# Performance work log

Hardware: AMD Instinct MI355X
Metric: run time of the kernel (lower is better)

## Reference

```python
import jax, jax.numpy as jnp
import numpy as np

N_NODES = 80000
N_EDGES = 1280000
D_NODE = 128
D_EDGE = 32
HID = 64
OUT = 32
EPS_GEN = 1e-7
EPS_BN = 1e-5


def _lin_init(key, fan_in, fan_out):
    return (jax.random.normal(key, (fan_in, fan_out), jnp.float32) / np.sqrt(fan_in))


def setup_inputs() -> dict:
    key = jax.random.key(0)
    ks = jax.random.split(key, 20)
    inp = {
        "x": jax.random.normal(ks[0], (N_NODES, D_NODE), jnp.float32),
        "edge_index": jax.random.randint(ks[1], (2, N_EDGES), 0, N_NODES, jnp.int32),
        "edge_attr": jax.random.normal(ks[2], (N_EDGES, D_EDGE), jnp.float32),
        # encoders
        "node_W": _lin_init(ks[3], D_NODE, HID), "node_b": jnp.zeros((HID,), jnp.float32),
        "edge_W": _lin_init(ks[4], D_EDGE, HID), "edge_b": jnp.zeros((HID,), jnp.float32),
        # GENConv layer 1 MLP: [HID -> 2HID (bias=False)] -> BN -> ReLU -> [2HID -> HID (bias=False)]
        "c1_W1": _lin_init(ks[5], HID, 2 * HID), "c1_g": jnp.ones((2 * HID,), jnp.float32), "c1_be": jnp.zeros((2 * HID,), jnp.float32), "c1_W2": _lin_init(ks[6], 2 * HID, HID),
        # GENConv layer 2
        "c2_W1": _lin_init(ks[7], HID, 2 * HID), "c2_g": jnp.ones((2 * HID,), jnp.float32), "c2_be": jnp.zeros((2 * HID,), jnp.float32), "c2_W2": _lin_init(ks[8], 2 * HID, HID),
        # edge update linears on concat(3*HID)
        "l1_W": _lin_init(ks[9], 3 * HID, HID), "l1_b": jnp.zeros((HID,), jnp.float32),
        "l2_W": _lin_init(ks[10], 3 * HID, OUT), "l2_b": jnp.zeros((OUT,), jnp.float32),
    }
    return inp


def _scatter_softmax_agg(msg, dst, n_nodes):
    # SoftmaxAggregation with t=1: per-destination, per-feature softmax weights
    m = jax.ops.segment_max(msg, dst, num_segments=n_nodes)  # [N, H]
    m = jnp.where(jnp.isfinite(m), m, 0.0)                   # nodes w/o in-edges
    ex = jnp.exp(msg - m[dst])                               # [E, H]
    denom = jax.ops.segment_sum(ex, dst, num_segments=n_nodes)
    alpha = ex / (denom[dst] + 1e-16)
    return jax.ops.segment_sum(msg * alpha, dst, num_segments=n_nodes)


def _batchnorm(h, gamma, beta):
    mu = jnp.mean(h, axis=0)
    var = jnp.var(h, axis=0)
    return (h - mu) * jax.lax.rsqrt(var + EPS_BN) * gamma + beta


def _genconv(x, src, dst, edge_attr, W1, g, be, W2):
    msg = jax.nn.relu(x[src] + edge_attr) + EPS_GEN          # [E, HID]
    agg = _scatter_softmax_agg(msg, dst, x.shape[0])         # [N, HID]
    h = agg + x
    h = jax.nn.relu(_batchnorm(h @ W1, g, be))
    return h @ W2


def reference(x, edge_index, edge_attr, node_W, node_b, edge_W, edge_b,
              c1_W1, c1_g, c1_be, c1_W2, c2_W1, c2_g, c2_be, c2_W2,
              l1_W, l1_b, l2_W, l2_b):
    src, dst = edge_index[0], edge_index[1]
    ea = edge_attr @ edge_W + edge_b                          # [E, HID]
    h = x @ node_W + node_b                                   # [N, HID]

    convs = [(c1_W1, c1_g, c1_be, c1_W2), (c2_W1, c2_g, c2_be, c2_W2)]
    lins = [(l1_W, l1_b), (l2_W, l2_b)]
    for (W1, g, be, W2), (lW, lb) in zip(convs, lins):
        h = jax.nn.relu(_genconv(h, src, dst, ea, W1, g, be, W2))
        # dropout is identity in eval mode
        ef = jnp.concatenate([h[src], ea, h[dst]], axis=-1)   # [E, 3*HID]
        ea = ef @ lW + lb
    return h, ea
```

## Files before the change

### kernel.cpp

```cpp
#include <hip/hip_runtime.h>
#include <hip/hip_bf16.h>

#define N_NODES 80000
#define N_EDGES 1280000
constexpr int DN = 128;
constexpr int DE = 32;
constexpr int H  = 64;
constexpr int H2 = 128;
constexpr float EPS_GEN = 1e-7f;
constexpr float EPS_BN  = 1e-5f;

typedef _Float16 f16x8 __attribute__((ext_vector_type(8)));
typedef _Float16 f16x4 __attribute__((ext_vector_type(4)));
typedef float f32x4 __attribute__((ext_vector_type(4)));

__device__ __forceinline__ void atomAddF(float* p, float v) {
  __hip_atomic_fetch_add(p, v, __ATOMIC_RELAXED, __HIP_MEMORY_SCOPE_AGENT);
}

struct PrepDesc { const float* W; _Float16* img; int K; int OC; int blkStart; };
struct PrepAll { PrepDesc d[8]; };

__global__ void k_prep_all(PrepAll P) {
  int b = blockIdx.x;
  int i = 0;
#pragma unroll
  for (int t = 1; t < 8; ++t)
    if (P.d[t].blkStart <= b) i = t;
  const PrepDesc D = P.d[i];
  int idx = (b - D.blkStart) * 256 + threadIdx.x;
  if (idx >= D.K * D.OC) return;
  int nslabK = D.K >> 5;
  int j = idx & 7, m16 = (idx >> 3) & 15, kg = (idx >> 7) & 3;
  int slab = idx >> 9;
  int kk = slab % nslabK, n2 = slab / nslabK;
  int k = kk * 32 + kg * 8 + j, n = n2 * 16 + m16;
  D.img[idx] = (_Float16)D.W[k * D.OC + n];
}

template <int K, int OC, bool IN16, bool AFFINE, bool BIAS,
          bool RELU_OUT, bool OUT16, bool OUT32, bool CLRS, bool SCATOUT>
__global__ __launch_bounds__(256) void k_dense(
    const void* __restrict__ Ain, const _Float16* __restrict__ wimg,
    const float* __restrict__ bias, const float* __restrict__ sums,
    const float* __restrict__ g, const float* __restrict__ be,
    const int* __restrict__ posmap,
    _Float16* __restrict__ out16, float* __restrict__ out32,
    float* __restrict__ sums_clr) {
  constexpr int NK = K / 32, NF = OC / 16;
  __shared__ float sSC[H2], sSH[H2];
  const int tid = threadIdx.x, wv = tid >> 6, lane = tid & 63;
  const int m16 = lane & 15, kg = lane >> 4;
  const int rowbase = blockIdx.x * 64 + wv * 16;
  if constexpr (CLRS) {
    if (blockIdx.x == 0) sums_clr[tid] = 0.0f;
  }
  if constexpr (AFFINE) {
    for (int i = tid; i < H2; i += 256) {
      float mu  = sums[i] * (1.0f / N_NODES);
      float var = sums[H2 + i] * (1.0f / N_NODES) - mu * mu;
      float sc  = rsqrtf(var + EPS_BN) * g[i];
      sSC[i] = sc;
      sSH[i] = be[i] - mu * sc;
    }
    __syncthreads();
  }
  const int arow = rowbase + m16;
  f32x4 acc[NF];
#pragma unroll
  for (int n2 = 0; n2 < NF; ++n2) {
    float bv = BIAS ? bias[n2 * 16 + m16] : 0.0f;
    acc[n2] = (f32x4){bv, bv, bv, bv};
  }
  const _Float16* wp = wimg + (size_t)lane * 8;
#pragma unroll
  for (int kk = 0; kk < NK; ++kk) {
    f16x8 a;
    if constexpr (IN16) {
      const _Float16* ap = (const _Float16*)Ain + (size_t)arow * K + kg * 8 + kk * 32;
      a = *(const f16x8*)ap;
      if constexpr (AFFINE) {
#pragma unroll
        for (int j = 0; j < 8; ++j) {
          int f = kg * 8 + kk * 32 + j;
          float v = fmaxf(fmaf((float)a[j], sSC[f], sSH[f]), 0.0f);
          a[j] = (_Float16)v;
        }
      }
    } else {
      const float* ap = (const float*)Ain + (size_t)arow * K + kg * 8 + kk * 32;
      float4 v0 = *(const float4*)ap;
      float4 v1 = *(const float4*)(ap + 4);
      a = (f16x8){(_Float16)v0.x, (_Float16)v0.y, (_Float16)v0.z, (_Float16)v0.w,
                  (_Float16)v1.x, (_Float16)v1.y, (_Float16)v1.z, (_Float16)v1.w};
    }
#pragma unroll
    for (int n2 = 0; n2 < NF; ++n2) {
      f16x8 bb = *(const f16x8*)(wp + ((size_t)(n2 * NK + kk) << 9));
      acc[n2] = __builtin_amdgcn_mfma_f32_16x16x32_f16(a, bb, acc[n2], 0, 0, 0);
    }
  }
#pragma unroll
  for (int n2 = 0; n2 < NF; ++n2)
#pragma unroll
    for (int r = 0; r < 4; ++r) {
      float o = acc[n2][r];
      if constexpr (RELU_OUT) o = fmaxf(o, 0.0f);
      int orow = rowbase + kg * 4 + r;
      if constexpr (SCATOUT) orow = posmap[orow];
      size_t oi = (size_t)orow * OC + n2 * 16 + m16;
      if constexpr (OUT16) out16[oi] = (_Float16)o;
      if constexpr (OUT32) out32[oi] = o;
    }
}

template <int OC, typename OUT_T, int T, bool SCAT>
__global__ __launch_bounds__(256) void k_edge_upd_srt(
    const _Float16* __restrict__ h, const _Float16* __restrict__ ea,
    const int2* __restrict__ eids, const int* __restrict__ dstS,
    const _Float16* __restrict__ wimg, const float* __restrict__ lb,
    OUT_T* __restrict__ eout) {
  constexpr int NF = OC / 16;
  __shared__ _Float16 sWf[NF * 6 * 512];
  __shared__ int sS[T * 64], sD[T * 64];
  __shared__ int sE[SCAT ? T * 64 : 1];
  const int tid = threadIdx.x, wv = tid >> 6, lane = tid & 63;
  const int m16 = lane & 15, kg = lane >> 4;
  const int p0 = blockIdx.x * (T * 64);

  for (int i = tid; i < T * 64; i += 256) {
    int2 t = eids[p0 + i];
    sS[i] = t.y;
    sD[i] = dstS[p0 + i];
    if constexpr (SCAT) sE[i] = t.x;
  }
  {
    const float4* s4 = (const float4*)wimg;
    float4* d4 = (float4*)sWf;
    constexpr int NV = NF * 6 * 512 / 8;
    for (int i = tid; i < NV; i += 256) d4[i] = s4[i];
  }
  __syncthreads();
  const _Float16* wp = sWf + (size_t)lane * 8;

  float bias_[NF];
#pragma unroll
  for (int n2 = 0; n2 < NF; ++n2) bias_[n2] = lb[n2 * 16 + m16];

  f16x8 FA[6], FB[6];
  auto LOADA = [&](f16x8* F, int l) {
    const _Float16* a0 = h + (size_t)sS[l] * H + kg * 8;
    const _Float16* a1 = ea + (size_t)(p0 + l) * H + kg * 8;
    const _Float16* a2 = h + (size_t)sD[l] * H + kg * 8;
    F[0] = *(const f16x8*)a0;
    F[1] = *(const f16x8*)(a0 + 32);
    F[2] = *(const f16x8*)a1;
    F[3] = *(const f16x8*)(a1 + 32);
    F[4] = *(const f16x8*)a2;
    F[5] = *(const f16x8*)(a2 + 32);
  };
  auto COMPUTE = [&](const f16x8* F, int l) {
    f32x4 acc[NF];
#pragma unroll
    for (int n2 = 0; n2 < NF; ++n2)
      acc[n2] = (f32x4){bias_[n2], bias_[n2], bias_[n2], bias_[n2]};
#pragma unroll
    for (int kk = 0; kk < 6; ++kk)
#pragma unroll
      for (int n2 = 0; n2 < NF; ++n2) {
        f16x8 bb = *(const f16x8*)(wp + ((n2 * 6 + kk) << 9));
        acc[n2] = __builtin_amdgcn_mfma_f32_16x16x32_f16(F[kk], bb, acc[n2], 0, 0, 0);
      }
    const int lbase = l - m16;
#pragma unroll
    for (int n2 = 0; n2 < NF; ++n2)
#pragma unroll
      for (int r = 0; r < 4; ++r) {
        int lr = lbase + kg * 4 + r;
        int col = n2 * 16 + m16;
        if constexpr (SCAT)
          eout[(size_t)sE[lr] * OC + col] = (OUT_T)acc[n2][r];
        else
          eout[(size_t)(p0 + lr) * OC + col] = (OUT_T)acc[n2][r];
      }
  };

  const int l0 = wv * 16 + m16;
  LOADA(FA, l0);
  if (T > 1) LOADA(FB, l0 + 64);
#pragma unroll
  for (int t = 0; t < T; ++t) {
    if (t & 1) {
      COMPUTE(FB, l0 + t * 64);
      if (t + 2 < T) LOADA(FB, l0 + (t + 2) * 64);
    } else {
      COMPUTE(FA, l0 + t * 64);
      if (t + 2 < T) LOADA(FA, l0 + (t + 2) * 64);
    }
  }
}

__global__ void k_hist(const int* __restrict__ dst, int* cnt) {
  int e = blockIdx.x * blockDim.x + threadIdx.x;
  if (e < N_EDGES) atomicAdd(&cnt[dst[e]], 1);
}

__global__ void k_scan_blk(const int* __restrict__ cnt, int* __restrict__ bsum) {
  __shared__ int sh[256];
  int i = blockIdx.x * 256 + threadIdx.x;
  sh[threadIdx.x] = (i < N_NODES) ? cnt[i] : 0;
  __syncthreads();
  for (int s = 128; s > 0; s >>= 1) {
    if (threadIdx.x < s) sh[threadIdx.x] += sh[threadIdx.x + s];
    __syncthreads();
  }
  if (threadIdx.x == 0) bsum[blockIdx.x] = sh[0];
}

__global__ void k_scan_top(int* bsum, int nb) {
  __shared__ int sh[512];
  int t = threadIdx.x;
  int orig = (t < nb) ? bsum[t] : 0;
  sh[t] = orig;
  __syncthreads();
  for (int off = 1; off < 512; off <<= 1) {
    int v = (t >= off) ? sh[t - off] : 0;
    __syncthreads();
    sh[t] += v;
    __syncthreads();
  }
  if (t < nb) bsum[t] = sh[t] - orig;
}

__global__ void k_scan_fin(const int* __restrict__ cnt, const int* __restrict__ bsum,
                           int* __restrict__ start, int* __restrict__ cursor) {
  __shared__ int sh[256];
  int i = blockIdx.x * 256 + threadIdx.x;
  int t = threadIdx.x;
  int orig = (i < N_NODES) ? cnt[i] : 0;
  sh[t] = orig;
  __syncthreads();
  for (int off = 1; off < 256; off <<= 1) {
    int v = (t >= off) ? sh[t - off] : 0;
    __syncthreads();
    sh[t] += v;
    __syncthreads();
  }
  if (i < N_NODES) {
    int st = bsum[blockIdx.x] + sh[t] - orig;
    start[i] = st;
    cursor[i] = st;
  }
}

__global__ void k_scatter(const int* __restrict__ src, const int* __restrict__ dst,
                          int* cursor, int2* __restrict__ eids, int* __restrict__ dstS,
                          int* __restrict__ posOf) {
  int e = blockIdx.x * blockDim.x + threadIdx.x;
  if (e < N_EDGES) {
    int d = dst[e];
    int pos = atomicAdd(&cursor[d], 1);
    eids[pos] = make_int2(e, src[e]);
    dstS[pos] = d;
    posOf[e] = pos;
  }
}

__global__ __launch_bounds__(256) void k_agg_csr(
    const _Float16* __restrict__ h, const _Float16* __restrict__ ea_s,
    const int2* __restrict__ eids, const int* __restrict__ start,
    const int* __restrict__ cnt, _Float16* __restrict__ hsum) {
  const int lane = threadIdx.x & 63;
  const int wid  = (int)((blockIdx.x * blockDim.x + threadIdx.x) >> 6);
  if (wid >= N_NODES) return;
  const int ep = lane >> 3, fg = lane & 7;
  const int s0 = start[wid], c = cnt[wid];
  float num[8] = {0.f, 0.f, 0.f, 0.f, 0.f, 0.f, 0.f, 0.f};
  float den[8] = {0.f, 0.f, 0.f, 0.f, 0.f, 0.f, 0.f, 0.f};
  if (c > 0) {
    const int nit = (c + 7) >> 3;
    int idx = min(ep, c - 1);
    f16x8 hA = *(const f16x8*)(h + (size_t)eids[s0 + idx].y * H + fg * 8);
    f16x8 eA = *(const f16x8*)(ea_s + (size_t)(s0 + idx) * H + fg * 8);
    bool vA = (ep < c);
    f16x8 hB = hA, eB = eA;
    bool vB = false;
    if (nit > 1) {
      idx = min(8 + ep, c - 1);
      hB = *(const f16x8*)(h + (size_t)eids[s0 + idx].y * H + fg * 8);
      eB = *(const f16x8*)(ea_s + (size_t)(s0 + idx) * H + fg * 8);
      vB = (8 + ep < c);
    }
    for (int i = 0; i < nit; ++i) {
      f16x8 hc = hA, ec = eA;
      bool vc = vA;
      hA = hB; eA = eB; vA = vB;
      if (i + 2 < nit) {
        idx = min((i + 2) * 8 + ep, c - 1);
        hB = *(const f16x8*)(h + (size_t)eids[s0 + idx].y * H + fg * 8);
        eB = *(const f16x8*)(ea_s + (size_t)(s0 + idx) * H + fg * 8);
        vB = ((i + 2) * 8 + ep < c);
      }
#pragma unroll
      for (int j = 0; j < 8; ++j) {
        float m = fmaxf((float)hc[j] + (float)ec[j], 0.0f) + EPS_GEN;
        float ex = vc ? __expf(m) : 0.0f;
        num[j] = fmaf(m, ex, num[j]);
        den[j] += ex;
      }
    }
  }
#pragma unroll
  for (int j = 0; j < 8; ++j) {
    num[j] += __shfl_xor(num[j], 8);
    num[j] += __shfl_xor(num[j], 16);
    num[j] += __shfl_xor(num[j], 32);
    den[j] += __shfl_xor(den[j], 8);
    den[j] += __shfl_xor(den[j], 16);
    den[j] += __shfl_xor(den[j], 32);
  }
  if (ep == 0) {
    f16x8 hs = *(const f16x8*)(h + (size_t)wid * H + fg * 8);
    f16x8 o;
#pragma unroll
    for (int j = 0; j < 8; ++j)
      o[j] = (_Float16)(num[j] / (den[j] + 1e-16f) + (float)hs[j]);
    *(f16x8*)(hsum + (size_t)wid * H + fg * 8) = o;
  }
}

__global__ void k_bnstats(const _Float16* __restrict__ h3, float* sums) {
  int f = threadIdx.x & (H2 - 1);
  int half = threadIdx.x >> 7;
  float s = 0.0f, q = 0.0f;
  for (int n = blockIdx.x * 2 + half; n < N_NODES; n += gridDim.x * 2) {
    float v = (float)h3[(size_t)n * H2 + f];
    s += v;
    q = fmaf(v, v, q);
  }
  __shared__ float sh[2][2][H2];
  sh[0][half][f] = s;
  sh[1][half][f] = q;
  __syncthreads();
  if (threadIdx.x < H2) {
    atomAddF(&sums[f], sh[0][0][f] + sh[0][1][f]);
    atomAddF(&sums[H2 + f], sh[1][0][f] + sh[1][1][f]);
  }
}

extern "C" void kernel_launch(void* const* d_in, const int* in_sizes, int n_in,
                              void* d_out, int out_size, void* d_ws, size_t ws_size,
                              hipStream_t stream) {
  (void)in_sizes; (void)n_in; (void)out_size; (void)ws_size;
  const float* x      = (const float*)d_in[0];
  const int*   eidx   = (const int*)d_in[1];
  const float* eattr  = (const float*)d_in[2];
  const float* node_W = (const float*)d_in[3];
  const float* node_b = (const float*)d_in[4];
  const float* edge_W = (const float*)d_in[5];
  const float* edge_b = (const float*)d_in[6];
  const float* c1_W1  = (const float*)d_in[7];
  const float* c1_g   = (const float*)d_in[8];
  const float* c1_be  = (const float*)d_in[9];
  const float* c1_W2  = (const float*)d_in[10];
  const float* c2_W1  = (const float*)d_in[11];
  const float* c2_g   = (const float*)d_in[12];
  const float* c2_be  = (const float*)d_in[13];
  const float* c2_W2  = (const float*)d_in[14];
  const float* l1_W   = (const float*)d_in[15];
  const float* l1_b   = (const float*)d_in[16];
  const float* l2_W   = (const float*)d_in[17];
  const float* l2_b   = (const float*)d_in[18];

  const int* src = eidx;
  const int* dst = eidx + N_EDGES;

  char* wsb = (char*)d_ws;
  size_t off = 0;
  _Float16* ea_s  = (_Float16*)(wsb + off); off += (size_t)N_EDGES * H * 2;
  _Float16* hA16  = (_Float16*)(wsb + off); off += (size_t)N_NODES * H * 2;
  _Float16* hB16  = (_Float16*)(wsb + off); off += (size_t)N_NODES * H * 2;
  _Float16* hC16  = (_Float16*)(wsb + off); off += (size_t)N_NODES * H * 2;
  _Float16* hsum16= (_Float16*)(wsb + off); off += (size_t)N_NODES * H * 2;
  _Float16* h3    = (_Float16*)(wsb + off); off += (size_t)N_NODES * H2 * 2;
  float* sums     = (float*)(wsb + off);    off += 256 * 4;
  int* cnt        = (int*)(wsb + off);      off += (size_t)N_NODES * 4;
  int* startA     = (int*)(wsb + off);      off += (size_t)N_NODES * 4;
  int* cursor     = (int*)(wsb + off);      off += (size_t)N_NODES * 4;
  int* bsum       = (int*)(wsb + off);      off += 512 * 4;
  int2* eids      = (int2*)(wsb + off);     off += (size_t)N_EDGES * 8;
  int* dstS       = (int*)(wsb + off);      off += (size_t)N_EDGES * 4;
  int* posOf      = (int*)(wsb + off);      off += (size_t)N_EDGES * 4;
  _Float16* wE    = (_Float16*)(wsb + off); off += DE * H * 2;
  _Float16* wN    = (_Float16*)(wsb + off); off += DN * H * 2;
  _Float16* w1a   = (_Float16*)(wsb + off); off += H * H2 * 2;
  _Float16* w1b   = (_Float16*)(wsb + off); off += H * H2 * 2;
  _Float16* w2a   = (_Float16*)(wsb + off); off += H2 * H * 2;
  _Float16* w2b   = (_Float16*)(wsb + off); off += H2 * H * 2;
  _Float16* wL1   = (_Float16*)(wsb + off); off += 3 * H * H * 2;
  _Float16* wL2   = (_Float16*)(wsb + off); off += 3 * H * 32 * 2;

  float* h_out  = (float*)d_out;
  float* ea_out = (float*)d_out + (size_t)N_NODES * H;

  constexpr int NB = (N_NODES + 255) / 256;

  PrepAll P;
  P.d[0] = {edge_W, wE, DE, H, 0};
  P.d[1] = {node_W, wN, DN, H, 8};
  P.d[2] = {c1_W1, w1a, H, H2, 40};
  P.d[3] = {c2_W1, w1b, H, H2, 72};
  P.d[4] = {c1_W2, w2a, H2, H, 104};
  P.d[5] = {c2_W2, w2b, H2, H, 136};
  P.d[6] = {l1_W, wL1, 192, H, 168};
  P.d[7] = {l2_W, wL2, 192, 32, 216};
  k_prep_all<<<240, 256, 0, stream>>>(P);

  hipMemsetAsync(cnt, 0, N_NODES * 4, stream);
  k_hist<<<(N_EDGES + 255) / 256, 256, 0, stream>>>(dst, cnt);
  k_scan_blk<<<NB, 256, 0, stream>>>(cnt, bsum);
  k_scan_top<<<1, 512, 0, stream>>>(bsum, NB);
  k_scan_fin<<<NB, 256, 0, stream>>>(cnt, bsum, startA, cursor);
  k_scatter<<<(N_EDGES + 255) / 256, 256, 0, stream>>>(src, dst, cursor, eids, dstS, posOf);

  k_dense<DE, H, false, false, true, false, true, false, false, true>
      <<<N_EDGES / 64, 256, 0, stream>>>(eattr, wE, edge_b, nullptr, nullptr, nullptr,
                                         posOf, ea_s, nullptr, nullptr);
  k_dense<DN, H, false, false, true, false, true, false, false, false>
      <<<N_NODES / 64, 256, 0, stream>>>(x, wN, node_b, nullptr, nullptr, nullptr,
                                         nullptr, hA16, nullptr, nullptr);

  k_agg_csr<<<(N_NODES + 3) / 4, 256, 0, stream>>>(hA16, ea_s, eids, startA, cnt, hsum16);
  k_dense<H, H2, true, false, false, false, true, false, true, false>
      <<<N_NODES / 64, 256, 0, stream>>>(hsum16, w1a, nullptr, nullptr, nullptr, nullptr,
                                         nullptr, h3, nullptr, sums);
  k_bnstats<<<1280, 256, 0, stream>>>(h3, sums);
  k_dense<H2, H, true, true, false, true, true, false, false, false>
      <<<N_NODES / 64, 256, 0, stream>>>(h3, w2a, nullptr, sums, c1_g, c1_be,
                                         nullptr, hB16, nullptr, nullptr);
  k_edge_upd_srt<64, _Float16, 8, false>
      <<<N_EDGES / 512, 256, 0, stream>>>(hB16, ea_s, eids, dstS, wL1, l1_b, ea_s);

  k_agg_csr<<<(N_NODES + 3) / 4, 256, 0, stream>>>(hB16, ea_s, eids, startA, cnt, hsum16);
  k_dense<H, H2, true, false, false, false, true, false, true, false>
      <<<N_NODES / 64, 256, 0, stream>>>(hsum16, w1b, nullptr, nullptr, nullptr, nullptr,
                                         nullptr, h3, nullptr, sums);
  k_bnstats<<<1280, 256, 0, stream>>>(h3, sums);
  k_dense<H2, H, true, true, false, true, true, true, false, false>
      <<<N_NODES / 64, 256, 0, stream>>>(h3, w2b, nullptr, sums, c2_g, c2_be,
                                         nullptr, hC16, h_out, nullptr);
  k_edge_upd_srt<32, float, 8, true>
      <<<N_EDGES / 512, 256, 0, stream>>>(hC16, ea_s, eids, dstS, wL2, l2_b, ea_out);
}
```

Before: 685.4 us.

## Fuse BatchNorm statistics into first GEMM and pack edge ids into int4

After: 663.9 us. -3.1%, faster.

```diff
diff --git a/kernel.cpp b/kernel.cpp
--- a/kernel.cpp
+++ b/kernel.cpp
@@ -39,22 +39,20 @@
 }
 
 template <int K, int OC, bool IN16, bool AFFINE, bool BIAS,
-          bool RELU_OUT, bool OUT16, bool OUT32, bool CLRS, bool SCATOUT>
+          bool RELU_OUT, bool OUT16, bool OUT32, bool SCATOUT, bool STATS>
 __global__ __launch_bounds__(256) void k_dense(
     const void* __restrict__ Ain, const _Float16* __restrict__ wimg,
     const float* __restrict__ bias, const float* __restrict__ sums,
     const float* __restrict__ g, const float* __restrict__ be,
     const int* __restrict__ posmap,
     _Float16* __restrict__ out16, float* __restrict__ out32,
-    float* __restrict__ sums_clr) {
+    float* __restrict__ sums_out) {
   constexpr int NK = K / 32, NF = OC / 16;
-  __shared__ float sSC[H2], sSH[H2];
+  __shared__ float sSC[AFFINE ? H2 : 1], sSH[AFFINE ? H2 : 1];
+  __shared__ float sStat[STATS ? 1024 : 1];
   const int tid = threadIdx.x, wv = tid >> 6, lane = tid & 63;
   const int m16 = lane & 15, kg = lane >> 4;
   const int rowbase = blockIdx.x * 64 + wv * 16;
-  if constexpr (CLRS) {
-    if (blockIdx.x == 0) sums_clr[tid] = 0.0f;
-  }
   if constexpr (AFFINE) {
     for (int i = tid; i < H2; i += 256) {
       float mu  = sums[i] * (1.0f / N_NODES);
@@ -112,12 +110,34 @@
       if constexpr (OUT16) out16[oi] = (_Float16)o;
       if constexpr (OUT32) out32[oi] = o;
     }
+  if constexpr (STATS) {
+    static_assert(!STATS || NF == 8, "STATS assumes OC==128");
+#pragma unroll
+    for (int n2 = 0; n2 < NF; ++n2) {
+      float s = acc[n2][0] + acc[n2][1] + acc[n2][2] + acc[n2][3];
+      float q = acc[n2][0] * acc[n2][0] + acc[n2][1] * acc[n2][1] +
+                acc[n2][2] * acc[n2][2] + acc[n2][3] * acc[n2][3];
+      s += __shfl_xor(s, 16); s += __shfl_xor(s, 32);
+      q += __shfl_xor(q, 16); q += __shfl_xor(q, 32);
+      if (kg == 0) {
+        sStat[wv * 128 + n2 * 16 + m16] = s;
+        sStat[512 + wv * 128 + n2 * 16 + m16] = q;
+      }
+    }
+    __syncthreads();
+    {
+      int which = tid >> 7, f = tid & 127;
+      const float* b0 = sStat + which * 512;
+      float v = b0[f] + b0[128 + f] + b0[256 + f] + b0[384 + f];
+      atomAddF(&sums_out[which * H2 + f], v);
+    }
+  }
 }
 
 template <int OC, typename OUT_T, int T, bool SCAT>
 __global__ __launch_bounds__(256) void k_edge_upd_srt(
     const _Float16* __restrict__ h, const _Float16* __restrict__ ea,
-    const int2* __restrict__ eids, const int* __restrict__ dstS,
+    const int4* __restrict__ eidsQ,
     const _Float16* __restrict__ wimg, const float* __restrict__ lb,
     OUT_T* __restrict__ eout) {
   constexpr int NF = OC / 16;
@@ -129,9 +149,9 @@
   const int p0 = blockIdx.x * (T * 64);
 
   for (int i = tid; i < T * 64; i += 256) {
-    int2 t = eids[p0 + i];
+    int4 t = eidsQ[p0 + i];
     sS[i] = t.y;
-    sD[i] = dstS[p0 + i];
+    sD[i] = t.z;
     if constexpr (SCAT) sE[i] = t.x;
   }
   {
@@ -254,22 +274,23 @@
 }
 
 __global__ void k_scatter(const int* __restrict__ src, const int* __restrict__ dst,
-                          int* cursor, int2* __restrict__ eids, int* __restrict__ dstS,
-                          int* __restrict__ posOf) {
+                          int* cursor, int4* __restrict__ eidsQ, int* __restrict__ posOf) {
   int e = blockIdx.x * blockDim.x + threadIdx.x;
   if (e < N_EDGES) {
     int d = dst[e];
+    int s = src[e];
     int pos = atomicAdd(&cursor[d], 1);
-    eids[pos] = make_int2(e, src[e]);
-    dstS[pos] = d;
+    eidsQ[pos] = make_int4(e, s, d, 0);
     posOf[e] = pos;
   }
 }
 
 __global__ __launch_bounds__(256) void k_agg_csr(
     const _Float16* __restrict__ h, const _Float16* __restrict__ ea_s,
-    const int2* __restrict__ eids, const int* __restrict__ start,
-    const int* __restrict__ cnt, _Float16* __restrict__ hsum) {
+    const int4* __restrict__ eidsQ, const int* __restrict__ start,
+    const int* __restrict__ cnt, _Float16* __restrict__ hsum,
+    float* __restrict__ sums_clr) {
+  if (blockIdx.x == 0) sums_clr[threadIdx.x] = 0.0f;
   const int lane = threadIdx.x & 63;
   const int wid  = (int)((blockIdx.x * blockDim.x + threadIdx.x) >> 6);
   if (wid >= N_NODES) return;
@@ -280,14 +301,16 @@
   if (c > 0) {
     const int nit = (c + 7) >> 3;
     int idx = min(ep, c - 1);
-    f16x8 hA = *(const f16x8*)(h + (size_t)eids[s0 + idx].y * H + fg * 8);
+    int2 pe = *(const int2*)(eidsQ + s0 + idx);
+    f16x8 hA = *(const f16x8*)(h + (size_t)pe.y * H + fg * 8);
     f16x8 eA = *(const f16x8*)(ea_s + (size_t)(s0 + idx) * H + fg * 8);
     bool vA = (ep < c);
     f16x8 hB = hA, eB = eA;
     bool vB = false;
     if (nit > 1) {
       idx = min(8 + ep, c - 1);
-      hB = *(const f16x8*)(h + (size_t)eids[s0 + idx].y * H + fg * 8);
+      pe = *(const int2*)(eidsQ + s0 + idx);
+      hB = *(const f16x8*)(h + (size_t)pe.y * H + fg * 8);
       eB = *(const f16x8*)(ea_s + (size_t)(s0 + idx) * H + fg * 8);
       vB = (8 + ep < c);
     }
@@ -297,7 +320,8 @@
       hA = hB; eA = eB; vA = vB;
       if (i + 2 < nit) {
         idx = min((i + 2) * 8 + ep, c - 1);
-        hB = *(const f16x8*)(h + (size_t)eids[s0 + idx].y * H + fg * 8);
+        pe = *(const int2*)(eidsQ + s0 + idx);
+        hB = *(const f16x8*)(h + (size_t)pe.y * H + fg * 8);
         eB = *(const f16x8*)(ea_s + (size_t)(s0 + idx) * H + fg * 8);
         vB = ((i + 2) * 8 + ep < c);
       }
@@ -326,25 +350,6 @@
     for (int j = 0; j < 8; ++j)
       o[j] = (_Float16)(num[j] / (den[j] + 1e-16f) + (float)hs[j]);
     *(f16x8*)(hsum + (size_t)wid * H + fg * 8) = o;
-  }
-}
-
-__global__ void k_bnstats(const _Float16* __restrict__ h3, float* sums) {
-  int f = threadIdx.x & (H2 - 1);
-  int half = threadIdx.x >> 7;
-  float s = 0.0f, q = 0.0f;
-  for (int n = blockIdx.x * 2 + half; n < N_NODES; n += gridDim.x * 2) {
-    float v = (float)h3[(size_t)n * H2 + f];
-    s += v;
-    q = fmaf(v, v, q);
-  }
-  __shared__ float sh[2][2][H2];
-  sh[0][half][f] = s;
-  sh[1][half][f] = q;
-  __syncthreads();
-  if (threadIdx.x < H2) {
-    atomAddF(&sums[f], sh[0][0][f] + sh[0][1][f]);
-    atomAddF(&sums[H2 + f], sh[1][0][f] + sh[1][1][f]);
   }
 }
 
@@ -388,8 +393,7 @@
   int* startA     = (int*)(wsb + off);      off += (size_t)N_NODES * 4;
   int* cursor     = (int*)(wsb + off);      off += (size_t)N_NODES * 4;
   int* bsum       = (int*)(wsb + off);      off += 512 * 4;
-  int2* eids      = (int2*)(wsb + off);     off += (size_t)N_EDGES * 8;
-  int* dstS       = (int*)(wsb + off);      off += (size_t)N_EDGES * 4;
+  int4* eidsQ     = (int4*)(wsb + off);     off += (size_t)N_EDGES * 16;
   int* posOf      = (int*)(wsb + off);      off += (size_t)N_EDGES * 4;
   _Float16* wE    = (_Float16*)(wsb + off); off += DE * H * 2;
   _Float16* wN    = (_Float16*)(wsb + off); off += DN * H * 2;
@@ -421,34 +425,32 @@
   k_scan_blk<<<NB, 256, 0, stream>>>(cnt, bsum);
   k_scan_top<<<1, 512, 0, stream>>>(bsum, NB);
   k_scan_fin<<<NB, 256, 0, stream>>>(cnt, bsum, startA, cursor);
-  k_scatter<<<(N_EDGES + 255) / 256, 256, 0, stream>>>(src, dst, cursor, eids, dstS, posOf);
-
-  k_dense<DE, H, false, false, true, false, true, false, false, true>
+  k_scatter<<<(N_EDGES + 255) / 256, 256, 0, stream>>>(src, dst, cursor, eidsQ, posOf);
+
+  k_dense<DE, H, false, false, true, false, true, false, true, false>
       <<<N_EDGES / 64, 256, 0, stream>>>(eattr, wE, edge_b, nullptr, nullptr, nullptr,
                                          posOf, ea_s, nullptr, nullptr);
   k_dense<DN, H, false, false, true, false, true, false, false, false>
       <<<N_NODES / 64, 256, 0, stream>>>(x, wN, node_b, nullptr, nullptr, nullptr,
                                          nullptr, hA16, nullptr, nullptr);
 
-  k_agg_csr<<<(N_NODES + 3) / 4, 256, 0, stream>>>(hA16, ea_s, eids, startA, cnt, hsum16);
-  k_dense<H, H2, true, false, false, false, true, false, true, false>
+  k_agg_csr<<<(N_NODES + 3) / 4, 256, 0, stream>>>(hA16, ea_s, eidsQ, startA, cnt, hsum16, sums);
+  k_dense<H, H2, true, false, false, false, true, false, false, true>
       <<<N_NODES / 64, 256, 0, stream>>>(hsum16, w1a, nullptr, nullptr, nullptr, nullptr,
                                          nullptr, h3, nullptr, sums);
-  k_bnstats<<<1280, 256, 0, stream>>>(h3, sums);
   k_dense<H2, H, true, true, false, true, true, false, false, false>
       <<<N_NODES / 64, 256, 0, stream>>>(h3, w2a, nullptr, sums, c1_g, c1_be,
                                          nullptr, hB16, nullptr, nullptr);
   k_edge_upd_srt<64, _Float16, 8, false>
-      <<<N_EDGES / 512, 256, 0, stream>>>(hB16, ea_s, eids, dstS, wL1, l1_b, ea_s);
-
-  k_agg_csr<<<(N_NODES + 3) / 4, 256, 0, stream>>>(hB16, ea_s, eids, startA, cnt, hsum16);
-  k_dense<H, H2, true, false, false, false, true, false, true, false>
+      <<<N_EDGES / 512, 256, 0, stream>>>(hB16, ea_s, eidsQ, wL1, l1_b, ea_s);
+
+  k_agg_csr<<<(N_NODES + 3) / 4, 256, 0, stream>>>(hB16, ea_s, eidsQ, startA, cnt, hsum16, sums);
+  k_dense<H, H2, true, false, false, false, true, false, false, true>
       <<<N_NODES / 64, 256, 0, stream>>>(hsum16, w1b, nullptr, nullptr, nullptr, nullptr,
                                          nullptr, h3, nullptr, sums);
-  k_bnstats<<<1280, 256, 0, stream>>>(h3, sums);
   k_dense<H2, H, true, true, false, true, true, true, false, false>
       <<<N_NODES / 64, 256, 0, stream>>>(h3, w2b, nullptr, sums, c2_g, c2_be,
                                          nullptr, hC16, h_out, nullptr);
   k_edge_upd_srt<32, float, 8, true>
-      <<<N_EDGES / 512, 256, 0, stream>>>(hC16, ea_s, eids, dstS, wL2, l2_b, ea_out);
-}
+      <<<N_EDGES / 512, 256, 0, stream>>>(hC16, ea_s, eidsQ, wL2, l2_b, ea_out);
+}
```
